# Performance work log

Measured on AMD Instinct MI355X. Metric: run time of the kernel, lower is better.

## Reference

```python
import jax, jax.numpy as jnp
import numpy as np

RATIO = 0.9375  # config.ratio


def setup_inputs() -> dict:
    key = jax.random.key(0)
    x = jax.random.normal(key, (4096, 8192), dtype=jnp.float32)
    return {"x": x}


def reference(x):
    # recall_window(x, ratio, dim=-1, keepdim=False)
    # For each row: sort, then find the minimum-length window covering
    # target = int(ratio * N) consecutive sorted values; return (left, right).
    N = x.shape[-1]
    target = int(RATIO * N)
    s = jnp.sort(x, axis=-1)                       # [R, N]
    # window_length[i] = s[i + target - 1] - s[i], for i in [0, N - target]
    lengths = s[:, target - 1:] - s[:, : N - target + 1]   # [R, N - target + 1]
    idx = jnp.argmin(lengths, axis=-1)             # first min, matches '<' in loop
    left = jnp.take_along_axis(s, idx[:, None], axis=-1)[:, 0]
    right = jnp.take_along_axis(s, (idx + target - 1)[:, None], axis=-1)[:, 0]
    return left, right
```

## Files before the change

kernel.cpp:

```cpp
#include <hip/hip_runtime.h>
#include <stdint.h>

#define ROWS   4096
#define NCOL   8192
#define TARGET 7680
#define NW     (NCOL - TARGET + 1)
#define NT     512
#define VPT    (NCOL / NT)
#define NB     2048
#define BPT    (NB / NT)
#define NWAVE  (NT / 64)
#define SCAP   2048
#define MAXS   (SCAP / NT)

struct Smem {
    uint32_t hist[NB];
    float    sorted[SCAP];
    float    sorted2[SCAP];
    uint32_t wsum[NWAVE];
    uint32_t res[4];
    float    fmin[NWAVE], fmax[NWAVE];
};

__device__ __forceinline__ int bin1f(float v, float mn, float s) {
    int b = (int)((v - mn) * s);
    return b > NB - 1 ? NB - 1 : b;
}
__device__ __forceinline__ int HIX(int b) { return ((b & 3) << 9) | (b >> 2); }

__global__ __launch_bounds__(NT, 4)
void recall_window_kernel(const float* __restrict__ x, float* __restrict__ out) {
    __shared__ Smem sm;
    const int tid = threadIdx.x;
    const int row = blockIdx.x;
    const int lane = tid & 63, wid = tid >> 6;

    float v[VPT];
    float mn = __int_as_float(0x7F800000), mx = -mn;
    const float4* xv = (const float4*)(x + (size_t)row * NCOL);
    #pragma unroll
    for (int j = 0; j < VPT / 4; j++) {
        float4 t = xv[tid + j * NT];
        v[4 * j + 0] = t.x; v[4 * j + 1] = t.y;
        v[4 * j + 2] = t.z; v[4 * j + 3] = t.w;
        mn = fminf(mn, fminf(fminf(t.x, t.y), fminf(t.z, t.w)));
        mx = fmaxf(mx, fmaxf(fmaxf(t.x, t.y), fmaxf(t.z, t.w)));
    }

    #pragma unroll
    for (int off = 32; off > 0; off >>= 1) {
        mn = fminf(mn, __shfl_down(mn, off, 64));
        mx = fmaxf(mx, __shfl_down(mx, off, 64));
    }
    if (lane == 0) { sm.fmin[wid] = mn; sm.fmax[wid] = mx; }
    #pragma unroll
    for (int j = 0; j < BPT; j++) sm.hist[tid + j * NT] = 0;
    __syncthreads();
    #pragma unroll
    for (int w = 0; w < NWAVE; w++) {
        mn = fminf(mn, sm.fmin[w]);
        mx = fmaxf(mx, sm.fmax[w]);
    }

    if (!(mx > mn)) {
        if (tid == 0) { out[row] = mn; out[ROWS + row] = mn; }
        return;
    }
    const float scale1 = (float)NB / (mx - mn);

    uint32_t binPk[VPT / 2];
    #pragma unroll
    for (int j = 0; j < VPT; j += 2) {
        int b0 = bin1f(v[j],     mn, scale1);
        int b1 = bin1f(v[j + 1], mn, scale1);
        binPk[j >> 1] = (uint32_t)b0 | ((uint32_t)b1 << 16);
        atomicAdd(&sm.hist[HIX(b0)], 1u);
        atomicAdd(&sm.hist[HIX(b1)], 1u);
    }
    __syncthreads();

    uint32_t h[BPT], s0 = 0;
    #pragma unroll
    for (int j = 0; j < BPT; j++) { h[j] = sm.hist[(j << 9) | tid]; s0 += h[j]; }
    uint32_t sc = s0;
    #pragma unroll
    for (int off = 1; off < 64; off <<= 1) {
        uint32_t n = __shfl_up(sc, off, 64);
        if (lane >= off) sc += n;
    }
    if (lane == 63) sm.wsum[wid] = sc;
    __syncthreads();
    uint32_t woff = 0;
    #pragma unroll
    for (int w = 0; w < NWAVE; w++) if (w < wid) woff += sm.wsum[w];
    const uint32_t incl = sc + woff, excl = incl - s0;
    const uint32_t ka = NW - 1, kb = TARGET - 1;
    if (ka >= excl && ka < incl) {
        uint32_t c = excl; bool done = false;
        #pragma unroll
        for (int j = 0; j < BPT; j++) {
            if (!done) {
                if (ka < c + h[j]) {
                    sm.res[0] = (uint32_t)(tid * BPT + j);
                    sm.res[1] = c + h[j];
                    done = true;
                } else c += h[j];
            }
        }
    }
    if (kb >= excl && kb < incl) {
        uint32_t c = excl; bool done = false;
        #pragma unroll
        for (int j = 0; j < BPT; j++) {
            if (!done) {
                if (kb < c + h[j]) {
                    sm.res[2] = (uint32_t)(tid * BPT + j);
                    sm.res[3] = c;
                    done = true;
                } else c += h[j];
            }
        }
    }
    {
        uint32_t run = excl;
        #pragma unroll
        for (int j = 0; j < BPT; j++) { sm.hist[(j << 9) | tid] = run; run += h[j]; }
    }
    __syncthreads();
    const int      B_lo    = (int)sm.res[0];
    const uint32_t cntB    = sm.res[1];
    const int      B_hi    = (int)sm.res[2];
    const uint32_t topBase = sm.res[3];
    const uint32_t shiftT  = cntB - topBase;
    uint32_t tot = cntB + (uint32_t)NCOL - topBase;
    if (tot > SCAP) tot = SCAP;

    #pragma unroll
    for (int j = 0; j < VPT; j++) {
        int b = (int)((binPk[j >> 1] >> ((j & 1) * 16)) & 0xffffu);
        if (b <= B_lo || b >= B_hi) {
            uint32_t pos = atomicAdd(&sm.hist[HIX(b)], 1u);
            if (b >= B_hi) pos += shiftT;
            if (pos < SCAP) sm.sorted[pos] = v[j];
        }
    }
    __syncthreads();

    #pragma unroll
    for (int it = 0; it < MAXS; it++) {
        int s = tid + it * NT;
        if (s < (int)tot) {
            float vv = sm.sorted[s];
            int b = bin1f(vv, mn, scale1);
            uint32_t en = sm.hist[HIX(b)];
            uint32_t st;
            if (s < (int)cntB) {
                st = (b == 0) ? 0u : sm.hist[HIX(b - 1)];
            } else {
                st = (b == B_hi) ? topBase : sm.hist[HIX(b - 1)];
                st += shiftT; en += shiftT;
            }
            if (en > tot) en = tot;
            uint32_t r = 0;
            if (en - st > 1) {
                for (uint32_t q = st; q < en; q++) {
                    float u = sm.sorted[q];
                    r += (u < vv) || (u == vv && (int)q < s);
                }
            }
            uint32_t d = st + r;
            if (d < SCAP) sm.sorted2[d] = vv;
        }
    }
    __syncthreads();


    if (wid == 0) {
        const int topstart = (int)tot - NW;
        float lbest = __int_as_float(0x7F800000);
        int   lidx  = 0x7FFFFFFF;
        for (int i = lane; i < NW; i += 64) {
            float len = sm.sorted2[topstart + i] - sm.sorted2[i];
            if (len < lbest) { lbest = len; lidx = i; }
        }
        #pragma unroll
        for (int off = 32; off > 0; off >>= 1) {
            float v2 = __shfl_down(lbest, off, 64);
            int   i2 = __shfl_down(lidx,  off, 64);
            if (v2 < lbest || (v2 == lbest && i2 < lidx)) { lbest = v2; lidx = i2; }
        }
        if (lane == 0) {
            out[row]        = sm.sorted2[lidx];
            out[ROWS + row] = sm.sorted2[topstart + lidx];
        }
    }
}

extern "C" void kernel_launch(void* const* d_in, const int* in_sizes, int n_in,
                              void* d_out, int out_size, void* d_ws, size_t ws_size,
                              hipStream_t stream) {
    const float* x = (const float*)d_in[0];
    float* out = (float*)d_out;
    recall_window_kernel<<<ROWS, NT, 0, stream>>>(x, out);
}
```

Before: 190.3 us.

## Process two rows per block with interleaved phases to hide latency

Each block now handles two rows, interleaving every phase (load, histogram, scan, scatter, fixup) between them so the independent work of one row can overlap stalls of the other and the barriers are shared. Shared memory doubles per block and the launch bound drops to 2 blocks per CU, which doubles the register state per thread. The histogram also switches from the interleaved HIX bank-spread index to linear indexing with uint4 vector loads and stores in the scan, which may add LDS bank conflicts on atomics. The grid shrinks to half as many blocks.

```diff
diff --git a/kernel.cpp b/kernel.cpp
--- a/kernel.cpp
+++ b/kernel.cpp
@@ -12,8 +12,10 @@
 #define NWAVE  (NT / 64)
 #define SCAP   2048
 #define MAXS   (SCAP / NT)
-
-struct Smem {
+#define RPB    2
+#define GRID   (ROWS / RPB)
+
+struct Half {
     uint32_t hist[NB];
     float    sorted[SCAP];
     float    sorted2[SCAP];
@@ -22,66 +24,74 @@
     float    fmin[NWAVE], fmax[NWAVE];
 };
 
+struct RState {
+    float    v[VPT];
+    uint32_t binPk[VPT / 2];
+    float    mn, mx, scale1;
+    int      degen;
+    uint32_t h[BPT];
+    uint32_t s0, sc;
+    int      B_lo, B_hi;
+    uint32_t cntB, topBase, shiftT, tot;
+};
+
 __device__ __forceinline__ int bin1f(float v, float mn, float s) {
     int b = (int)((v - mn) * s);
     return b > NB - 1 ? NB - 1 : b;
 }
-__device__ __forceinline__ int HIX(int b) { return ((b & 3) << 9) | (b >> 2); }
-
-__global__ __launch_bounds__(NT, 4)
-void recall_window_kernel(const float* __restrict__ x, float* __restrict__ out) {
-    __shared__ Smem sm;
-    const int tid = threadIdx.x;
-    const int row = blockIdx.x;
-    const int lane = tid & 63, wid = tid >> 6;
-
-    float v[VPT];
-    float mn = __int_as_float(0x7F800000), mx = -mn;
+
+
+__device__ __forceinline__ void ph_load(const float* __restrict__ x, int row,
+                                        int tid, RState& r) {
     const float4* xv = (const float4*)(x + (size_t)row * NCOL);
     #pragma unroll
     for (int j = 0; j < VPT / 4; j++) {
         float4 t = xv[tid + j * NT];
-        v[4 * j + 0] = t.x; v[4 * j + 1] = t.y;
-        v[4 * j + 2] = t.z; v[4 * j + 3] = t.w;
-        mn = fminf(mn, fminf(fminf(t.x, t.y), fminf(t.z, t.w)));
-        mx = fmaxf(mx, fmaxf(fmaxf(t.x, t.y), fmaxf(t.z, t.w)));
-    }
-
+        r.v[4 * j + 0] = t.x; r.v[4 * j + 1] = t.y;
+        r.v[4 * j + 2] = t.z; r.v[4 * j + 3] = t.w;
+    }
+    float mn = r.v[0], mx = r.v[0];
+    #pragma unroll
+    for (int j = 1; j < VPT; j++) { mn = fminf(mn, r.v[j]); mx = fmaxf(mx, r.v[j]); }
+    r.mn = mn; r.mx = mx;
+}
+
+__device__ __forceinline__ void ph_wave_minmax(Half& sm, RState& r, int lane, int wid) {
+    float mn = r.mn, mx = r.mx;
     #pragma unroll
     for (int off = 32; off > 0; off >>= 1) {
         mn = fminf(mn, __shfl_down(mn, off, 64));
         mx = fmaxf(mx, __shfl_down(mx, off, 64));
     }
     if (lane == 0) { sm.fmin[wid] = mn; sm.fmax[wid] = mx; }
-    #pragma unroll
-    for (int j = 0; j < BPT; j++) sm.hist[tid + j * NT] = 0;
-    __syncthreads();
-    #pragma unroll
-    for (int w = 0; w < NWAVE; w++) {
-        mn = fminf(mn, sm.fmin[w]);
-        mx = fmaxf(mx, sm.fmax[w]);
-    }
-
-    if (!(mx > mn)) {
-        if (tid == 0) { out[row] = mn; out[ROWS + row] = mn; }
-        return;
-    }
-    const float scale1 = (float)NB / (mx - mn);
-
-    uint32_t binPk[VPT / 2];
+}
+
+__device__ __forceinline__ void ph_final_minmax(Half& sm, RState& r) {
+    float mn = sm.fmin[0], mx = sm.fmax[0];
+    #pragma unroll
+    for (int w = 1; w < NWAVE; w++) { mn = fminf(mn, sm.fmin[w]); mx = fmaxf(mx, sm.fmax[w]); }
+    r.mn = mn; r.mx = mx;
+    r.degen = !(mx > mn);
+    r.scale1 = r.degen ? 0.0f : (float)NB / (mx - mn);
+}
+
+__device__ __forceinline__ void ph_hist(Half& sm, RState& r) {
+    if (r.degen) return;
     #pragma unroll
     for (int j = 0; j < VPT; j += 2) {
-        int b0 = bin1f(v[j],     mn, scale1);
-        int b1 = bin1f(v[j + 1], mn, scale1);
-        binPk[j >> 1] = (uint32_t)b0 | ((uint32_t)b1 << 16);
-        atomicAdd(&sm.hist[HIX(b0)], 1u);
-        atomicAdd(&sm.hist[HIX(b1)], 1u);
-    }
-    __syncthreads();
-
-    uint32_t h[BPT], s0 = 0;
-    #pragma unroll
-    for (int j = 0; j < BPT; j++) { h[j] = sm.hist[(j << 9) | tid]; s0 += h[j]; }
+        int b0 = bin1f(r.v[j],     r.mn, r.scale1);
+        int b1 = bin1f(r.v[j + 1], r.mn, r.scale1);
+        r.binPk[j >> 1] = (uint32_t)b0 | ((uint32_t)b1 << 16);
+        atomicAdd(&sm.hist[b0], 1u);
+        atomicAdd(&sm.hist[b1], 1u);
+    }
+}
+
+__device__ __forceinline__ void ph_scan_pre(Half& sm, RState& r, int tid, int lane, int wid) {
+    if (r.degen) return;
+    uint4 hv = *(const uint4*)&sm.hist[tid * BPT];
+    r.h[0] = hv.x; r.h[1] = hv.y; r.h[2] = hv.z; r.h[3] = hv.w;
+    uint32_t s0 = hv.x + hv.y + hv.z + hv.w;
     uint32_t sc = s0;
     #pragma unroll
     for (int off = 1; off < 64; off <<= 1) {
@@ -89,22 +99,26 @@
         if (lane >= off) sc += n;
     }
     if (lane == 63) sm.wsum[wid] = sc;
-    __syncthreads();
+    r.s0 = s0; r.sc = sc;
+}
+
+__device__ __forceinline__ void ph_scan_post(Half& sm, RState& r, int tid, int wid) {
+    if (r.degen) return;
     uint32_t woff = 0;
     #pragma unroll
     for (int w = 0; w < NWAVE; w++) if (w < wid) woff += sm.wsum[w];
-    const uint32_t incl = sc + woff, excl = incl - s0;
+    const uint32_t incl = r.sc + woff, excl = incl - r.s0;
     const uint32_t ka = NW - 1, kb = TARGET - 1;
     if (ka >= excl && ka < incl) {
         uint32_t c = excl; bool done = false;
         #pragma unroll
         for (int j = 0; j < BPT; j++) {
             if (!done) {
-                if (ka < c + h[j]) {
+                if (ka < c + r.h[j]) {
                     sm.res[0] = (uint32_t)(tid * BPT + j);
-                    sm.res[1] = c + h[j];
+                    sm.res[1] = c + r.h[j];
                     done = true;
-                } else c += h[j];
+                } else c += r.h[j];
             }
         }
     }
@@ -113,87 +127,145 @@
         #pragma unroll
         for (int j = 0; j < BPT; j++) {
             if (!done) {
-                if (kb < c + h[j]) {
+                if (kb < c + r.h[j]) {
                     sm.res[2] = (uint32_t)(tid * BPT + j);
                     sm.res[3] = c;
                     done = true;
-                } else c += h[j];
-            }
-        }
-    }
-    {
-        uint32_t run = excl;
-        #pragma unroll
-        for (int j = 0; j < BPT; j++) { sm.hist[(j << 9) | tid] = run; run += h[j]; }
-    }
-    __syncthreads();
-    const int      B_lo    = (int)sm.res[0];
-    const uint32_t cntB    = sm.res[1];
-    const int      B_hi    = (int)sm.res[2];
-    const uint32_t topBase = sm.res[3];
-    const uint32_t shiftT  = cntB - topBase;
-    uint32_t tot = cntB + (uint32_t)NCOL - topBase;
-    if (tot > SCAP) tot = SCAP;
-
+                } else c += r.h[j];
+            }
+        }
+    }
+    uint4 w4;
+    uint32_t run = excl;
+    w4.x = run; run += r.h[0];
+    w4.y = run; run += r.h[1];
+    w4.z = run; run += r.h[2];
+    w4.w = run;
+    *(uint4*)&sm.hist[tid * BPT] = w4;
+}
+
+__device__ __forceinline__ void ph_getres(Half& sm, RState& r) {
+    if (r.degen) return;
+    r.B_lo = (int)sm.res[0]; r.cntB   = sm.res[1];
+    r.B_hi = (int)sm.res[2]; r.topBase = sm.res[3];
+    r.shiftT = r.cntB - r.topBase;
+    uint32_t tot = r.cntB + (uint32_t)NCOL - r.topBase;
+    r.tot = tot > SCAP ? SCAP : tot;
+}
+
+__device__ __forceinline__ void ph_scatter(Half& sm, RState& r) {
+    if (r.degen) return;
     #pragma unroll
     for (int j = 0; j < VPT; j++) {
-        int b = (int)((binPk[j >> 1] >> ((j & 1) * 16)) & 0xffffu);
-        if (b <= B_lo || b >= B_hi) {
-            uint32_t pos = atomicAdd(&sm.hist[HIX(b)], 1u);
-            if (b >= B_hi) pos += shiftT;
-            if (pos < SCAP) sm.sorted[pos] = v[j];
-        }
-    }
-    __syncthreads();
-
+        int b = (int)((r.binPk[j >> 1] >> ((j & 1) * 16)) & 0xffffu);
+        if (b <= r.B_lo || b >= r.B_hi) {
+            uint32_t pos = atomicAdd(&sm.hist[b], 1u);
+            if (b >= r.B_hi) pos += r.shiftT;
+            if (pos < SCAP) sm.sorted[pos] = r.v[j];
+        }
+    }
+}
+
+__device__ __forceinline__ void ph_fixup(Half& sm, RState& r, int tid) {
+    if (r.degen) return;
     #pragma unroll
     for (int it = 0; it < MAXS; it++) {
         int s = tid + it * NT;
-        if (s < (int)tot) {
+        if (s < (int)r.tot) {
             float vv = sm.sorted[s];
-            int b = bin1f(vv, mn, scale1);
-            uint32_t en = sm.hist[HIX(b)];
+            int b = bin1f(vv, r.mn, r.scale1);
+            uint32_t en = sm.hist[b];
             uint32_t st;
-            if (s < (int)cntB) {
-                st = (b == 0) ? 0u : sm.hist[HIX(b - 1)];
+            if (s < (int)r.cntB) {
+                st = (b == 0) ? 0u : sm.hist[b - 1];
             } else {
-                st = (b == B_hi) ? topBase : sm.hist[HIX(b - 1)];
-                st += shiftT; en += shiftT;
-            }
-            if (en > tot) en = tot;
-            uint32_t r = 0;
+                st = (b == r.B_hi) ? r.topBase : sm.hist[b - 1];
+                st += r.shiftT; en += r.shiftT;
+            }
+            if (en > r.tot) en = r.tot;
+            uint32_t rr = 0;
             if (en - st > 1) {
                 for (uint32_t q = st; q < en; q++) {
                     float u = sm.sorted[q];
-                    r += (u < vv) || (u == vv && (int)q < s);
+                    rr += (u < vv) || (u == vv && (int)q < s);
                 }
             }
-            uint32_t d = st + r;
+            uint32_t d = st + rr;
             if (d < SCAP) sm.sorted2[d] = vv;
         }
     }
-    __syncthreads();
-
-
-    if (wid == 0) {
-        const int topstart = (int)tot - NW;
-        float lbest = __int_as_float(0x7F800000);
-        int   lidx  = 0x7FFFFFFF;
-        for (int i = lane; i < NW; i += 64) {
-            float len = sm.sorted2[topstart + i] - sm.sorted2[i];
-            if (len < lbest) { lbest = len; lidx = i; }
-        }
-        #pragma unroll
-        for (int off = 32; off > 0; off >>= 1) {
-            float v2 = __shfl_down(lbest, off, 64);
-            int   i2 = __shfl_down(lidx,  off, 64);
-            if (v2 < lbest || (v2 == lbest && i2 < lidx)) { lbest = v2; lidx = i2; }
-        }
-        if (lane == 0) {
-            out[row]        = sm.sorted2[lidx];
-            out[ROWS + row] = sm.sorted2[topstart + lidx];
-        }
-    }
+}
+
+__device__ __forceinline__ void ph_argmin(Half& sm, RState& r, int row, int lane,
+                                          float* __restrict__ out) {
+    if (r.degen) {
+        if (lane == 0) { out[row] = r.mn; out[ROWS + row] = r.mn; }
+        return;
+    }
+    const int topstart = (int)r.tot - NW;
+    float lbest = __int_as_float(0x7F800000);
+    int   lidx  = 0x7FFFFFFF;
+    for (int i = lane; i < NW; i += 64) {
+        float len = sm.sorted2[topstart + i] - sm.sorted2[i];
+        if (len < lbest) { lbest = len; lidx = i; }
+    }
+    #pragma unroll
+    for (int off = 32; off > 0; off >>= 1) {
+        float v2 = __shfl_down(lbest, off, 64);
+        int   i2 = __shfl_down(lidx,  off, 64);
+        if (v2 < lbest || (v2 == lbest && i2 < lidx)) { lbest = v2; lidx = i2; }
+    }
+    if (lane == 0) {
+        out[row]        = sm.sorted2[lidx];
+        out[ROWS + row] = sm.sorted2[topstart + lidx];
+    }
+}
+
+__global__ __launch_bounds__(NT, 2)
+void recall_window_kernel(const float* __restrict__ x, float* __restrict__ out) {
+    __shared__ Half smA, smB;
+    const int tid = threadIdx.x;
+    const int lane = tid & 63, wid = tid >> 6;
+    const int rowA = blockIdx.x * RPB, rowB = rowA + 1;
+    RState ra, rb;
+
+    ph_load(x, rowA, tid, ra);
+    ph_load(x, rowB, tid, rb);
+    ph_wave_minmax(smA, ra, lane, wid);
+    ph_wave_minmax(smB, rb, lane, wid);
+    #pragma unroll
+    for (int j = 0; j < BPT; j++) {
+        smA.hist[tid + j * NT] = 0;
+        smB.hist[tid + j * NT] = 0;
+    }
+    __syncthreads();
+    ph_final_minmax(smA, ra);
+    ph_final_minmax(smB, rb);
+
+    ph_hist(smA, ra);
+    ph_hist(smB, rb);
+    __syncthreads();
+
+    ph_scan_pre(smA, ra, tid, lane, wid);
+    ph_scan_pre(smB, rb, tid, lane, wid);
+    __syncthreads();
+
+    ph_scan_post(smA, ra, tid, wid);
+    ph_scan_post(smB, rb, tid, wid);
+    __syncthreads();
+
+    ph_getres(smA, ra);
+    ph_getres(smB, rb);
+    ph_scatter(smA, ra);
+    ph_scatter(smB, rb);
+    __syncthreads();
+
+    ph_fixup(smA, ra, tid);
+    ph_fixup(smB, rb, tid);
+    __syncthreads();
+
+    if (wid == 0)      ph_argmin(smA, ra, rowA, lane, out);
+    else if (wid == 1) ph_argmin(smB, rb, rowB, lane, out);
 }
 
 extern "C" void kernel_launch(void* const* d_in, const int* in_sizes, int n_in,
@@ -201,5 +273,5 @@
                               hipStream_t stream) {
     const float* x = (const float*)d_in[0];
     float* out = (float*)d_out;
-    recall_window_kernel<<<ROWS, NT, 0, stream>>>(x, out);
-}
+    recall_window_kernel<<<GRID, NT, 0, stream>>>(x, out);
+}
```

New measurement: 207.6 us. 9.1% more time.

## Use a fixed histogram range with fallback, and locate bins by binary search

Applied to the files above, without the earlier changes.

Drops the per-row min/max reduction and its barrier by binning values into a fixed range of [-16, 16], with the binning folded into the global-load loop. If the selected tail buckets overflow the shared buffer, the kernel recomputes the true range and re-histograms. In the ranking stage each sorted value's bucket is now found by binary search over the prefix offsets rather than recomputed from the value. In exchange, the bins are coarser for the normal test data, and the binary search adds LDS reads per element.

```diff
diff --git a/kernel.cpp b/kernel.cpp
--- a/kernel.cpp
+++ b/kernel.cpp
@@ -12,6 +12,8 @@
 #define NWAVE  (NT / 64)
 #define SCAP   2048
 #define MAXS   (SCAP / NT)
+#define FMN    (-16.0f)
+#define FSC    ((float)NB / 32.0f)
 
 struct Smem {
     uint32_t hist[NB];
@@ -22,78 +24,63 @@
     float    fmin[NWAVE], fmax[NWAVE];
 };
 
-__device__ __forceinline__ int bin1f(float v, float mn, float s) {
+__device__ __forceinline__ int binf(float v, float mn, float s) {
     int b = (int)((v - mn) * s);
+    b = b < 0 ? 0 : b;
     return b > NB - 1 ? NB - 1 : b;
 }
 __device__ __forceinline__ int HIX(int b) { return ((b & 3) << 9) | (b >> 2); }
 
-__global__ __launch_bounds__(NT, 4)
-void recall_window_kernel(const float* __restrict__ x, float* __restrict__ out) {
-    __shared__ Smem sm;
-    const int tid = threadIdx.x;
-    const int row = blockIdx.x;
-    const int lane = tid & 63, wid = tid >> 6;
-
-    float v[VPT];
-    float mn = __int_as_float(0x7F800000), mx = -mn;
-    const float4* xv = (const float4*)(x + (size_t)row * NCOL);
-    #pragma unroll
-    for (int j = 0; j < VPT / 4; j++) {
-        float4 t = xv[tid + j * NT];
-        v[4 * j + 0] = t.x; v[4 * j + 1] = t.y;
-        v[4 * j + 2] = t.z; v[4 * j + 3] = t.w;
-        mn = fminf(mn, fminf(fminf(t.x, t.y), fminf(t.z, t.w)));
-        mx = fmaxf(mx, fmaxf(fmaxf(t.x, t.y), fmaxf(t.z, t.w)));
-    }
-
-    #pragma unroll
-    for (int off = 32; off > 0; off >>= 1) {
-        mn = fminf(mn, __shfl_down(mn, off, 64));
-        mx = fmaxf(mx, __shfl_down(mx, off, 64));
-    }
-    if (lane == 0) { sm.fmin[wid] = mn; sm.fmax[wid] = mx; }
-    #pragma unroll
-    for (int j = 0; j < BPT; j++) sm.hist[tid + j * NT] = 0;
-    __syncthreads();
-    #pragma unroll
-    for (int w = 0; w < NWAVE; w++) {
-        mn = fminf(mn, sm.fmin[w]);
-        mx = fmaxf(mx, sm.fmax[w]);
-    }
-
-    if (!(mx > mn)) {
-        if (tid == 0) { out[row] = mn; out[ROWS + row] = mn; }
-        return;
-    }
-    const float scale1 = (float)NB / (mx - mn);
-
-    uint32_t binPk[VPT / 2];
-    #pragma unroll
-    for (int j = 0; j < VPT; j += 2) {
-        int b0 = bin1f(v[j],     mn, scale1);
-        int b1 = bin1f(v[j + 1], mn, scale1);
-        binPk[j >> 1] = (uint32_t)b0 | ((uint32_t)b1 << 16);
-        atomicAdd(&sm.hist[HIX(b0)], 1u);
-        atomicAdd(&sm.hist[HIX(b1)], 1u);
+struct P1Out { int B_lo, B_hi; uint32_t cntB, topBase, shiftT, tot; };
+
+template<bool LOAD>
+__device__ __forceinline__ void phase1(Smem& sm, const float* __restrict__ xrow,
+                                       float (&v)[VPT], uint32_t (&binPk)[VPT / 2],
+                                       float mn, float sc,
+                                       int tid, int lane, int wid, P1Out& o) {
+    if (LOAD) {
+        const float4* xv = (const float4*)xrow;
+        #pragma unroll
+        for (int q = 0; q < VPT / 4; q++) {
+            float4 t = xv[tid + q * NT];
+            v[4 * q + 0] = t.x; v[4 * q + 1] = t.y;
+            v[4 * q + 2] = t.z; v[4 * q + 3] = t.w;
+            int b0 = binf(t.x, mn, sc), b1 = binf(t.y, mn, sc);
+            int b2 = binf(t.z, mn, sc), b3 = binf(t.w, mn, sc);
+            binPk[2 * q + 0] = (uint32_t)b0 | ((uint32_t)b1 << 16);
+            binPk[2 * q + 1] = (uint32_t)b2 | ((uint32_t)b3 << 16);
+            atomicAdd(&sm.hist[HIX(b0)], 1u);
+            atomicAdd(&sm.hist[HIX(b1)], 1u);
+            atomicAdd(&sm.hist[HIX(b2)], 1u);
+            atomicAdd(&sm.hist[HIX(b3)], 1u);
+        }
+    } else {
+        #pragma unroll
+        for (int j = 0; j < VPT; j += 2) {
+            int b0 = binf(v[j],     mn, sc);
+            int b1 = binf(v[j + 1], mn, sc);
+            binPk[j >> 1] = (uint32_t)b0 | ((uint32_t)b1 << 16);
+            atomicAdd(&sm.hist[HIX(b0)], 1u);
+            atomicAdd(&sm.hist[HIX(b1)], 1u);
+        }
     }
     __syncthreads();
 
     uint32_t h[BPT], s0 = 0;
     #pragma unroll
     for (int j = 0; j < BPT; j++) { h[j] = sm.hist[(j << 9) | tid]; s0 += h[j]; }
-    uint32_t sc = s0;
+    uint32_t sc2 = s0;
     #pragma unroll
     for (int off = 1; off < 64; off <<= 1) {
-        uint32_t n = __shfl_up(sc, off, 64);
-        if (lane >= off) sc += n;
-    }
-    if (lane == 63) sm.wsum[wid] = sc;
+        uint32_t n = __shfl_up(sc2, off, 64);
+        if (lane >= off) sc2 += n;
+    }
+    if (lane == 63) sm.wsum[wid] = sc2;
     __syncthreads();
     uint32_t woff = 0;
     #pragma unroll
     for (int w = 0; w < NWAVE; w++) if (w < wid) woff += sm.wsum[w];
-    const uint32_t incl = sc + woff, excl = incl - s0;
+    const uint32_t incl = sc2 + woff, excl = incl - s0;
     const uint32_t ka = NW - 1, kb = TARGET - 1;
     if (ka >= excl && ka < incl) {
         uint32_t c = excl; bool done = false;
@@ -127,13 +114,64 @@
         for (int j = 0; j < BPT; j++) { sm.hist[(j << 9) | tid] = run; run += h[j]; }
     }
     __syncthreads();
-    const int      B_lo    = (int)sm.res[0];
-    const uint32_t cntB    = sm.res[1];
-    const int      B_hi    = (int)sm.res[2];
-    const uint32_t topBase = sm.res[3];
-    const uint32_t shiftT  = cntB - topBase;
-    uint32_t tot = cntB + (uint32_t)NCOL - topBase;
-    if (tot > SCAP) tot = SCAP;
+    o.B_lo = (int)sm.res[0]; o.cntB    = sm.res[1];
+    o.B_hi = (int)sm.res[2]; o.topBase = sm.res[3];
+    o.shiftT = o.cntB - o.topBase;
+    o.tot = o.cntB + (uint32_t)NCOL - o.topBase;
+}
+
+__global__ __launch_bounds__(NT, 4)
+void recall_window_kernel(const float* __restrict__ x, float* __restrict__ out) {
+    __shared__ Smem sm;
+    const int tid = threadIdx.x;
+    const int row = blockIdx.x;
+    const int lane = tid & 63, wid = tid >> 6;
+
+    {
+        uint4 z; z.x = 0; z.y = 0; z.z = 0; z.w = 0;
+        *(uint4*)&sm.hist[tid * 4] = z;
+    }
+    __syncthreads();
+
+    float    v[VPT];
+    uint32_t binPk[VPT / 2];
+    P1Out    o;
+    phase1<true>(sm, x + (size_t)row * NCOL, v, binPk, FMN, FSC,
+                 tid, lane, wid, o);
+
+    if (o.tot > SCAP) {
+        float mn = v[0], mx = v[0];
+        #pragma unroll
+        for (int j = 1; j < VPT; j++) { mn = fminf(mn, v[j]); mx = fmaxf(mx, v[j]); }
+        #pragma unroll
+        for (int off = 32; off > 0; off >>= 1) {
+            mn = fminf(mn, __shfl_down(mn, off, 64));
+            mx = fmaxf(mx, __shfl_down(mx, off, 64));
+        }
+        if (lane == 0) { sm.fmin[wid] = mn; sm.fmax[wid] = mx; }
+        {
+            uint4 z; z.x = 0; z.y = 0; z.z = 0; z.w = 0;
+            *(uint4*)&sm.hist[tid * 4] = z;
+        }
+        __syncthreads();
+        #pragma unroll
+        for (int w = 0; w < NWAVE; w++) {
+            mn = fminf(mn, sm.fmin[w]);
+            mx = fmaxf(mx, sm.fmax[w]);
+        }
+        if (!(mx > mn)) {
+            if (tid == 0) { out[row] = mn; out[ROWS + row] = mn; }
+            return;
+        }
+        phase1<false>(sm, nullptr, v, binPk, mn, (float)NB / (mx - mn),
+                      tid, lane, wid, o);
+        if (o.tot > SCAP) o.tot = SCAP;
+    }
+    const int      B_lo   = o.B_lo;
+    const int      B_hi   = o.B_hi;
+    const uint32_t cntB   = o.cntB, topBase = o.topBase, shiftT = o.shiftT;
+    const uint32_t tot    = o.tot;
+    const float    mnG    = FMN;
 
     #pragma unroll
     for (int j = 0; j < VPT; j++) {
@@ -146,30 +184,40 @@
     }
     __syncthreads();
 
-    #pragma unroll
-    for (int it = 0; it < MAXS; it++) {
-        int s = tid + it * NT;
-        if (s < (int)tot) {
-            float vv = sm.sorted[s];
-            int b = bin1f(vv, mn, scale1);
-            uint32_t en = sm.hist[HIX(b)];
-            uint32_t st;
-            if (s < (int)cntB) {
-                st = (b == 0) ? 0u : sm.hist[HIX(b - 1)];
-            } else {
-                st = (b == B_hi) ? topBase : sm.hist[HIX(b - 1)];
-                st += shiftT; en += shiftT;
+    {
+        #pragma unroll
+        for (int it = 0; it < MAXS; it++) {
+            int s = tid + it * NT;
+            if (s < (int)tot) {
+                float vv = sm.sorted[s];
+                bool bot = s < (int)cntB;
+                int lo = bot ? 0 : B_hi, hi = bot ? B_lo : NB - 1;
+                uint32_t su = bot ? (uint32_t)s : (uint32_t)s - shiftT;
+                while (lo < hi) {
+                    int mid = (lo + hi) >> 1;
+                    uint32_t en_m = sm.hist[HIX(mid)];
+                    if (su < en_m) hi = mid; else lo = mid + 1;
+                }
+                int b = lo;
+                uint32_t en = sm.hist[HIX(b)];
+                uint32_t st;
+                if (bot) {
+                    st = (b == 0) ? 0u : sm.hist[HIX(b - 1)];
+                } else {
+                    st = (b == B_hi) ? topBase : sm.hist[HIX(b - 1)];
+                    st += shiftT; en += shiftT;
+                }
+                if (en > tot) en = tot;
+                uint32_t r = 0;
+                if (en - st > 1) {
+                    for (uint32_t q = st; q < en; q++) {
+                        float u = sm.sorted[q];
+                        r += (u < vv) || (u == vv && (int)q < s);
+                    }
+                }
+                uint32_t d = st + r;
+                if (d < SCAP) sm.sorted2[d] = vv;
             }
-            if (en > tot) en = tot;
-            uint32_t r = 0;
-            if (en - st > 1) {
-                for (uint32_t q = st; q < en; q++) {
-                    float u = sm.sorted[q];
-                    r += (u < vv) || (u == vv && (int)q < s);
-                }
-            }
-            uint32_t d = st + r;
-            if (d < SCAP) sm.sorted2[d] = vv;
         }
     }
     __syncthreads();
@@ -194,6 +242,7 @@
             out[ROWS + row] = sm.sorted2[topstart + lidx];
         }
     }
+    (void)mnG;
 }
 
 extern "C" void kernel_launch(void* const* d_in, const int* in_sizes, int n_in,
```

After: 207.1 us. +8.8%, slower.

## Add fixed-threshold tail fast path that bins only the outer values

Applied to the files above, without the earlier changes.

Each row first counts values below and above fixed thresholds (±1.38) chosen to match the expected data distribution. If both tails hold enough elements for every candidate window and together fit the shared buffer, only those tail values are histogrammed, scattered and sorted, using fixed bin ranges. This skips the min/max reduction and the histogram atomics on the roughly 85% of values in the middle. Rows that fail the check fall back to the original exact path, now with vectorized histogram zeroing and bins recomputed instead of packed. Results stay exact for any input, but the speed gain depends on the test data being roughly standard normal.

```diff
diff --git a/kernel.cpp b/kernel.cpp
--- a/kernel.cpp
+++ b/kernel.cpp
@@ -13,20 +13,40 @@
 #define SCAP   2048
 #define MAXS   (SCAP / NT)
 
+#define T_LO   (-1.38f)
+#define T_HI   (1.38f)
+#define NBS    1024
+#define BMIN   (-4.0f)
+#define BSC    ((float)NBS / (T_LO - BMIN))
+
 struct Smem {
     uint32_t hist[NB];
     float    sorted[SCAP];
     float    sorted2[SCAP];
     uint32_t wsum[NWAVE];
+    uint32_t cntlo[NWAVE], cnthi[NWAVE];
     uint32_t res[4];
     float    fmin[NWAVE], fmax[NWAVE];
 };
 
-__device__ __forceinline__ int bin1f(float v, float mn, float s) {
+__device__ __forceinline__ int HIX(int b) { return ((b & 3) << 9) | (b >> 2); }
+
+__device__ __forceinline__ int bin_bot(float v) {
+    int b = (int)((v - BMIN) * BSC);
+    b = b < 0 ? 0 : b;
+    return b > NBS - 1 ? NBS - 1 : b;
+}
+__device__ __forceinline__ int bin_top(float v) {
+    int b = (int)((v - T_HI) * BSC);
+    b = b < 0 ? 0 : b;
+    b = b > NBS - 1 ? NBS - 1 : b;
+    return NBS + b;
+}
+__device__ __forceinline__ int binf(float v, float mn, float s) {
     int b = (int)((v - mn) * s);
+    b = b < 0 ? 0 : b;
     return b > NB - 1 ? NB - 1 : b;
 }
-__device__ __forceinline__ int HIX(int b) { return ((b & 3) << 9) | (b >> 2); }
 
 __global__ __launch_bounds__(NT, 4)
 void recall_window_kernel(const float* __restrict__ x, float* __restrict__ out) {
@@ -36,47 +56,146 @@
     const int lane = tid & 63, wid = tid >> 6;
 
     float v[VPT];
-    float mn = __int_as_float(0x7F800000), mx = -mn;
+    uint32_t clo = 0, chi = 0;
     const float4* xv = (const float4*)(x + (size_t)row * NCOL);
     #pragma unroll
     for (int j = 0; j < VPT / 4; j++) {
         float4 t = xv[tid + j * NT];
         v[4 * j + 0] = t.x; v[4 * j + 1] = t.y;
         v[4 * j + 2] = t.z; v[4 * j + 3] = t.w;
-        mn = fminf(mn, fminf(fminf(t.x, t.y), fminf(t.z, t.w)));
-        mx = fmaxf(mx, fmaxf(fmaxf(t.x, t.y), fmaxf(t.z, t.w)));
-    }
-
+        clo += (t.x < T_LO) + (t.y < T_LO) + (t.z < T_LO) + (t.w < T_LO);
+        chi += (t.x > T_HI) + (t.y > T_HI) + (t.z > T_HI) + (t.w > T_HI);
+    }
+    #pragma unroll
+    for (int off = 32; off > 0; off >>= 1) {
+        clo += __shfl_down(clo, off, 64);
+        chi += __shfl_down(chi, off, 64);
+    }
+    if (lane == 0) { sm.cntlo[wid] = clo; sm.cnthi[wid] = chi; }
+    {
+        uint4 z; z.x = 0; z.y = 0; z.z = 0; z.w = 0;
+        *(uint4*)&sm.hist[tid * 4] = z;
+    }
+    __syncthreads();
+    uint32_t cnt_lo = 0, cnt_hi = 0;
+    #pragma unroll
+    for (int w = 0; w < NWAVE; w++) { cnt_lo += sm.cntlo[w]; cnt_hi += sm.cnthi[w]; }
+    const uint32_t totF = cnt_lo + cnt_hi;
+    const bool fast = (cnt_lo >= NW) && (cnt_hi >= NW) && (totF <= SCAP);
+
+    if (fast) {
+        #pragma unroll
+        for (int j = 0; j < VPT; j++) {
+            float val = v[j];
+            bool bot = val < T_LO, top = val > T_HI;
+            if (bot | top) {
+                int b = bot ? bin_bot(val) : bin_top(val);
+                atomicAdd(&sm.hist[HIX(b)], 1u);
+            }
+        }
+        __syncthreads();
+
+        uint32_t h[BPT], s0 = 0;
+        #pragma unroll
+        for (int j = 0; j < BPT; j++) { h[j] = sm.hist[(j << 9) | tid]; s0 += h[j]; }
+        uint32_t sc = s0;
+        #pragma unroll
+        for (int off = 1; off < 64; off <<= 1) {
+            uint32_t n = __shfl_up(sc, off, 64);
+            if (lane >= off) sc += n;
+        }
+        if (lane == 63) sm.wsum[wid] = sc;
+        __syncthreads();
+        uint32_t woff = 0;
+        #pragma unroll
+        for (int w = 0; w < NWAVE; w++) if (w < wid) woff += sm.wsum[w];
+        uint32_t run = sc + woff - s0;
+        #pragma unroll
+        for (int j = 0; j < BPT; j++) { sm.hist[(j << 9) | tid] = run; run += h[j]; }
+        __syncthreads();
+
+        #pragma unroll
+        for (int j = 0; j < VPT; j++) {
+            float val = v[j];
+            bool bot = val < T_LO, top = val > T_HI;
+            if (bot | top) {
+                int b = bot ? bin_bot(val) : bin_top(val);
+                uint32_t pos = atomicAdd(&sm.hist[HIX(b)], 1u);
+                if (pos < SCAP) sm.sorted[pos] = val;
+            }
+        }
+        __syncthreads();
+
+        #pragma unroll
+        for (int it = 0; it < MAXS; it++) {
+            int s = tid + it * NT;
+            if (s < (int)totF) {
+                float vv = sm.sorted[s];
+                int b = (s < (int)cnt_lo) ? bin_bot(vv) : bin_top(vv);
+                uint32_t en = sm.hist[HIX(b)];
+                uint32_t st = (b == 0) ? 0u : sm.hist[HIX(b - 1)];
+                uint32_t r = 0;
+                if (en - st > 1) {
+                    for (uint32_t q = st; q < en; q++) {
+                        float u = sm.sorted[q];
+                        r += (u < vv) || (u == vv && (int)q < s);
+                    }
+                }
+                sm.sorted2[st + r] = vv;
+            }
+        }
+        __syncthreads();
+
+        if (wid == 0) {
+            const int topstart = (int)totF - NW;
+            float lbest = __int_as_float(0x7F800000);
+            int   lidx  = 0x7FFFFFFF;
+            for (int i = lane; i < NW; i += 64) {
+                float len = sm.sorted2[topstart + i] - sm.sorted2[i];
+                if (len < lbest) { lbest = len; lidx = i; }
+            }
+            #pragma unroll
+            for (int off = 32; off > 0; off >>= 1) {
+                float v2 = __shfl_down(lbest, off, 64);
+                int   i2 = __shfl_down(lidx,  off, 64);
+                if (v2 < lbest || (v2 == lbest && i2 < lidx)) { lbest = v2; lidx = i2; }
+            }
+            if (lane == 0) {
+                out[row]        = sm.sorted2[lidx];
+                out[ROWS + row] = sm.sorted2[topstart + lidx];
+            }
+        }
+        return;
+    }
+
+    float mn = v[0], mx = v[0];
+    #pragma unroll
+    for (int j = 1; j < VPT; j++) { mn = fminf(mn, v[j]); mx = fmaxf(mx, v[j]); }
     #pragma unroll
     for (int off = 32; off > 0; off >>= 1) {
         mn = fminf(mn, __shfl_down(mn, off, 64));
         mx = fmaxf(mx, __shfl_down(mx, off, 64));
     }
     if (lane == 0) { sm.fmin[wid] = mn; sm.fmax[wid] = mx; }
-    #pragma unroll
-    for (int j = 0; j < BPT; j++) sm.hist[tid + j * NT] = 0;
+    {
+        uint4 z; z.x = 0; z.y = 0; z.z = 0; z.w = 0;
+        *(uint4*)&sm.hist[tid * 4] = z;
+    }
     __syncthreads();
     #pragma unroll
     for (int w = 0; w < NWAVE; w++) {
         mn = fminf(mn, sm.fmin[w]);
         mx = fmaxf(mx, sm.fmax[w]);
     }
-
     if (!(mx > mn)) {
         if (tid == 0) { out[row] = mn; out[ROWS + row] = mn; }
         return;
     }
-    const float scale1 = (float)NB / (mx - mn);
-
-    uint32_t binPk[VPT / 2];
-    #pragma unroll
-    for (int j = 0; j < VPT; j += 2) {
-        int b0 = bin1f(v[j],     mn, scale1);
-        int b1 = bin1f(v[j + 1], mn, scale1);
-        binPk[j >> 1] = (uint32_t)b0 | ((uint32_t)b1 << 16);
-        atomicAdd(&sm.hist[HIX(b0)], 1u);
-        atomicAdd(&sm.hist[HIX(b1)], 1u);
-    }
+    const float amn = mn, asc = (float)NB / (mx - mn);
+
+    #pragma unroll
+    for (int j = 0; j < VPT; j++)
+        atomicAdd(&sm.hist[HIX(binf(v[j], amn, asc))], 1u);
     __syncthreads();
 
     uint32_t h[BPT], s0 = 0;
@@ -137,11 +256,12 @@
 
     #pragma unroll
     for (int j = 0; j < VPT; j++) {
-        int b = (int)((binPk[j >> 1] >> ((j & 1) * 16)) & 0xffffu);
+        float val = v[j];
+        int b = binf(val, amn, asc);
         if (b <= B_lo || b >= B_hi) {
             uint32_t pos = atomicAdd(&sm.hist[HIX(b)], 1u);
             if (b >= B_hi) pos += shiftT;
-            if (pos < SCAP) sm.sorted[pos] = v[j];
+            if (pos < SCAP) sm.sorted[pos] = val;
         }
     }
     __syncthreads();
@@ -151,7 +271,7 @@
         int s = tid + it * NT;
         if (s < (int)tot) {
             float vv = sm.sorted[s];
-            int b = bin1f(vv, mn, scale1);
+            int b = binf(vv, amn, asc);
             uint32_t en = sm.hist[HIX(b)];
             uint32_t st;
             if (s < (int)cntB) {
@@ -174,7 +294,6 @@
     }
     __syncthreads();
 
-
     if (wid == 0) {
         const int topstart = (int)tot - NW;
         float lbest = __int_as_float(0x7F800000);
```

Result: slower. 218.5 us (+14.8%).
